# Kernel optimization log

Hardware: AMD Instinct MI355X
Metric: run time of the kernel (lower is better)

Reference implementation:

```python
import jax, jax.numpy as jnp
import numpy as np

NUM_NODES = 200000   # graph size
E = 128              # embedding_size
B = 256              # batch of target nodes
M = 8                # num_metapaths
L = 64               # walk length (number of (n1,n2,e) triples per metapath)
NUM_EDGE_TYPE = 8
H = 8                # num_heads (hardcoded in module)


def setup_inputs() -> dict:
    key = jax.random.key(0)
    ks = jax.random.split(key, 10)
    # walks: last dim = (n1, n2, edge_type)
    n12 = jax.random.randint(ks[0], (B, M, L, 2), 0, NUM_NODES)
    ety = jax.random.randint(ks[1], (B, M, L, 1), 0, NUM_EDGE_TYPE)
    node_mp_walks = jnp.concatenate([n12, ety], axis=-1)
    node_idx = jax.random.randint(ks[2], (B,), 0, NUM_NODES)
    mp_type_idx = jnp.arange(M)
    # fc1(onehot(n)) == node_table[n] + fc1_b  (node_table = fc1.weight.T)
    node_table = jax.random.normal(ks[3], (NUM_NODES, E), dtype=jnp.float32) * 0.1
    fc1_b = jnp.zeros((E,), dtype=jnp.float32)
    edge_table = jax.random.normal(ks[4], (NUM_EDGE_TYPE, E), dtype=jnp.float32) * 0.1
    # Indexed_LinearFC_List: one (E,E) linear per metapath
    W_mp = jax.random.normal(ks[5], (M, E, E), dtype=jnp.float32) * 0.05
    b_mp = jnp.zeros((M, E), dtype=jnp.float32)
    # MultiheadAttention params (embed_dim=E, num_heads=H, eval mode -> no dropout)
    Wqkv = jax.random.normal(ks[6], (3 * E, E), dtype=jnp.float32) * 0.05
    bqkv = jnp.zeros((3 * E,), dtype=jnp.float32)
    Wo = jax.random.normal(ks[7], (E, E), dtype=jnp.float32) * 0.05
    bo = jnp.zeros((E,), dtype=jnp.float32)
    return dict(node_idx=node_idx, mp_type_idx=mp_type_idx, node_mp_walks=node_mp_walks,
                node_table=node_table, fc1_b=fc1_b, edge_table=edge_table,
                W_mp=W_mp, b_mp=b_mp, Wqkv=Wqkv, bqkv=bqkv, Wo=Wo, bo=bo)


def reference(node_idx, mp_type_idx, node_mp_walks, node_table, fc1_b, edge_table,
              W_mp, b_mp, Wqkv, bqkv, Wo, bo):
    n1 = node_mp_walks[..., 0]          # [B,M,L]
    n2 = node_mp_walks[..., 1]
    e = node_mp_walks[..., 2]
    # gather node/edge embeddings (fc1 over one-hot == table row + bias)
    n1_vec = node_table[n1] + fc1_b     # [B,M,L,E]
    n2_vec = node_table[n2] + fc1_b     # [B,M,L,E]
    edge_vec = edge_table[e]            # [B,M,L,E]
    # elementwise fuse + mean over walk steps
    mp_agg_0 = jnp.mean(n1_vec * n2_vec * edge_vec, axis=2)        # [B,M,E]
    # per-metapath indexed linear
    Wsel = W_mp[mp_type_idx]            # [M,E,E]
    bsel = b_mp[mp_type_idx]            # [M,E]
    mp_agg_1 = jnp.einsum('bme,meo->bmo', mp_agg_0, Wsel) + bsel   # [B,M,E]
    # self-attention over metapaths (torch MHA, seq-first layout: [M,B,E])
    x = jnp.transpose(mp_agg_1, (1, 0, 2))                         # [M,B,E]
    qkv = x @ Wqkv.T + bqkv                                        # [M,B,3E]
    q, k, v = jnp.split(qkv, 3, axis=-1)
    hd = E // H
    q = q.reshape(M, B, H, hd)
    k = k.reshape(M, B, H, hd)
    v = v.reshape(M, B, H, hd)
    scores = jnp.einsum('mbhd,nbhd->bhmn', q, k) / jnp.sqrt(jnp.float32(hd))
    attn = jax.nn.softmax(scores, axis=-1)                         # [B,H,M,M]
    o = jnp.einsum('bhmn,nbhd->mbhd', attn, v).reshape(M, B, E)
    attn_output = o @ Wo.T + bo                                    # [M,B,E]
    return attn_output
```

## Files before the change

kernel.cpp:

```cpp
#include <hip/hip_runtime.h>

#define B 256
#define M 8
#define L 64
#define E 128
#define H 8
#define HD 16
#define NET 8
#define E3 384

__global__ __launch_bounds__(256) void k_transpose(
    const float* __restrict__ Wqkv, const float* __restrict__ Wo,
    float* __restrict__ WqkvT, float* __restrict__ WoT) {
  int idx = blockIdx.x * 256 + threadIdx.x;
  if (idx < E * E3) {
    int e = idx / E3;
    int o = idx - e * E3;
    WqkvT[idx] = Wqkv[o * E + e];
  } else {
    int j = idx - E * E3;
    int e = j >> 7, o = j & 127;
    WoT[j] = Wo[o * E + e];
  }
}

__global__ __launch_bounds__(256) void k_gather(
    const int* __restrict__ walks, const float* __restrict__ node_table,
    const float* __restrict__ fc1_b, const float* __restrict__ edge_table,
    float* __restrict__ agg0) {
  __shared__ int s_idx[L * 3];
  __shared__ float s_et[NET * E];
  __shared__ float4 s_red[256];

  int r = blockIdx.x;
  int t = threadIdx.x;
  int g = t >> 5, lane = t & 31;

  if (t < L * 3) s_idx[t] = walks[r * (L * 3) + t];
  for (int i = t; i < NET * E; i += 256) s_et[i] = edge_table[i];
  __syncthreads();

  const float4* nt4 = (const float4*)node_table;
  float4 fb = ((const float4*)fc1_b)[lane];
  float4 acc = make_float4(0.f, 0.f, 0.f, 0.f);

  #pragma unroll
  for (int i = 0; i < 8; ++i) {
    int l = (i << 3) + g;
    int n1 = s_idx[3 * l];
    int n2 = s_idx[3 * l + 1];
    int et = s_idx[3 * l + 2];
    float4 a = nt4[n1 * 32 + lane];
    float4 c = nt4[n2 * 32 + lane];
    float4 ev = ((const float4*)(s_et + et * E))[lane];
    acc.x += (a.x + fb.x) * (c.x + fb.x) * ev.x;
    acc.y += (a.y + fb.y) * (c.y + fb.y) * ev.y;
    acc.z += (a.z + fb.z) * (c.z + fb.z) * ev.z;
    acc.w += (a.w + fb.w) * (c.w + fb.w) * ev.w;
  }
  s_red[t] = acc;
  __syncthreads();
  if (t < 32) {
    float4 s = s_red[t];
    #pragma unroll
    for (int gg = 1; gg < 8; ++gg) {
      float4 v = s_red[gg * 32 + t];
      s.x += v.x; s.y += v.y; s.z += v.z; s.w += v.w;
    }
    const float inv = 1.0f / (float)L;
    s.x *= inv; s.y *= inv; s.z *= inv; s.w *= inv;
    ((float4*)agg0)[r * 32 + t] = s;
  }
}

__global__ __launch_bounds__(256) void k_mlp(
    const float* __restrict__ agg0, const int* __restrict__ mp_type_idx,
    const float* __restrict__ W_mp, const float* __restrict__ b_mp,
    const float* __restrict__ WqkvT, const float* __restrict__ bqkv,
    float* __restrict__ qkv) {
  __shared__ float xs[8][E];
  __shared__ float ys[8][E];
  int t = threadIdx.x;
  int m = blockIdx.y;
  int b0 = blockIdx.x * 8;
  int mp = mp_type_idx[m];
  int o = t & 127;
  int half = t >> 7;

  #pragma unroll
  for (int i = 0; i < 4; ++i) {
    int idx = i * 256 + t;
    int j = idx >> 7, e = idx & 127;
    xs[j][e] = agg0[((b0 + j) * M + m) * E + e];
  }
  __syncthreads();

  {
    const float* W = W_mp + mp * E * E;
    float acc[4] = {0, 0, 0, 0};
    for (int e = 0; e < E; ++e) {
      float w = W[e * E + o];
      #pragma unroll
      for (int j = 0; j < 4; ++j) acc[j] += xs[half * 4 + j][e] * w;
    }
    float bias = b_mp[mp * E + o];
    #pragma unroll
    for (int j = 0; j < 4; ++j) ys[half * 4 + j][o] = acc[j] + bias;
  }
  __syncthreads();

  #pragma unroll
  for (int c = 0; c < 3; ++c) {
    int oc = c * E + o;
    float acc[4] = {0, 0, 0, 0};
    for (int e = 0; e < E; ++e) {
      float w = WqkvT[e * E3 + oc];
      #pragma unroll
      for (int j = 0; j < 4; ++j) acc[j] += ys[half * 4 + j][e] * w;
    }
    float bias = bqkv[oc];
    #pragma unroll
    for (int j = 0; j < 4; ++j)
      qkv[((b0 + half * 4 + j) * M + m) * E3 + oc] = acc[j] + bias;
  }
}

__global__ __launch_bounds__(256) void k_attn(
    const float* __restrict__ qkv, const float* __restrict__ WoT,
    const float* __restrict__ bo, float* __restrict__ out) {
  __shared__ float s_qkv[M][E3 + 1];
  __shared__ float s_sc[H][M][M];
  __shared__ float s_o[M][E];
  int b = blockIdx.x;
  int t = threadIdx.x;

  #pragma unroll
  for (int i = 0; i < 12; ++i) {
    int idx = i * 256 + t;
    int mt = idx / E3;
    int col = idx - mt * E3;
    s_qkv[mt][col] = qkv[(b * M + mt) * E3 + col];
  }
  __syncthreads();

  #pragma unroll
  for (int i = 0; i < 2; ++i) {
    int idx = i * 256 + t;
    int h = idx >> 6;
    int mq = (idx >> 3) & 7;
    int n = idx & 7;
    float s = 0.f;
    #pragma unroll
    for (int d = 0; d < HD; ++d)
      s += s_qkv[mq][h * HD + d] * s_qkv[n][E + h * HD + d];
    s_sc[h][mq][n] = s * 0.25f;
  }
  __syncthreads();

  if (t < 64) {
    int h = t >> 3, mq = t & 7;
    float mx = -1e30f;
    #pragma unroll
    for (int n = 0; n < 8; ++n) mx = fmaxf(mx, s_sc[h][mq][n]);
    float ex[8];
    float sum = 0.f;
    #pragma unroll
    for (int n = 0; n < 8; ++n) { ex[n] = __expf(s_sc[h][mq][n] - mx); sum += ex[n]; }
    float inv = 1.0f / sum;
    #pragma unroll
    for (int n = 0; n < 8; ++n) s_sc[h][mq][n] = ex[n] * inv;
  }
  __syncthreads();

  #pragma unroll
  for (int i = 0; i < 4; ++i) {
    int idx = i * 256 + t;
    int mq = idx >> 7;
    int col = idx & 127;
    int h = col >> 4;
    float s = 0.f;
    #pragma unroll
    for (int n = 0; n < 8; ++n)
      s += s_sc[h][mq][n] * s_qkv[n][2 * E + col];
    s_o[mq][col] = s;
  }
  __syncthreads();

  int o = t & 127;
  int mbase = t >> 7;
  float accp[4] = {0, 0, 0, 0};
  for (int e = 0; e < E; ++e) {
    float w = WoT[e * E + o];
    #pragma unroll
    for (int i = 0; i < 4; ++i)
      accp[i] += s_o[2 * i + mbase][e] * w;
  }
  float bias = bo[o];
  #pragma unroll
  for (int i = 0; i < 4; ++i) {
    int mq = 2 * i + mbase;
    out[(mq * B + b) * E + o] = accp[i] + bias;
  }
}

extern "C" void kernel_launch(void* const* d_in, const int* in_sizes, int n_in,
                              void* d_out, int out_size, void* d_ws, size_t ws_size,
                              hipStream_t stream) {
  const int*   mp_type_idx = (const int*)d_in[1];
  const int*   walks       = (const int*)d_in[2];
  const float* node_table  = (const float*)d_in[3];
  const float* fc1_b       = (const float*)d_in[4];
  const float* edge_table  = (const float*)d_in[5];
  const float* W_mp        = (const float*)d_in[6];
  const float* b_mp        = (const float*)d_in[7];
  const float* Wqkv        = (const float*)d_in[8];
  const float* bqkv        = (const float*)d_in[9];
  const float* Wo          = (const float*)d_in[10];
  const float* bo          = (const float*)d_in[11];
  float* out = (float*)d_out;

  char* ws = (char*)d_ws;
  float* agg0  = (float*)(ws);
  float* qkvb  = (float*)(ws + (1 << 20));
  float* WqkvT = (float*)(ws + (4 << 20));
  float* WoT   = (float*)(ws + (4 << 20) + (256 << 10));

  k_transpose<<<dim3(256), dim3(256), 0, stream>>>(Wqkv, Wo, WqkvT, WoT);
  k_gather<<<dim3(B * M), dim3(256), 0, stream>>>(walks, node_table, fc1_b, edge_table, agg0);
  k_mlp<<<dim3(32, 8), dim3(256), 0, stream>>>(agg0, mp_type_idx, W_mp, b_mp, WqkvT, bqkv, qkvb);
  k_attn<<<dim3(B), dim3(256), 0, stream>>>(qkvb, WoT, bo, out);
}
```

Before: 208.2 us.

## Fuse gather, metapath linear, QKV projection and attention into one kernel

Merges the gather/mean, per-metapath linear, QKV projection and attention/output projection into a single kernel with one block per batch element, keeping intermediates in shared memory. This removes global round trips for agg0 and qkv and two kernel launches. The gather loop is restructured to issue eight independent row loads per step, increasing memory-level parallelism per thread. The trade-off is far fewer blocks (one per batch item) for the bandwidth-bound gather, which may reduce latency hiding, plus repeated weight reads per block.

```diff
diff --git a/kernel.cpp b/kernel.cpp
--- a/kernel.cpp
+++ b/kernel.cpp
@@ -24,122 +24,93 @@
   }
 }
 
-__global__ __launch_bounds__(256) void k_gather(
+__global__ __launch_bounds__(256) void k_fused(
     const int* __restrict__ walks, const float* __restrict__ node_table,
     const float* __restrict__ fc1_b, const float* __restrict__ edge_table,
-    float* __restrict__ agg0) {
-  __shared__ int s_idx[L * 3];
+    const int* __restrict__ mp_type_idx,
+    const float* __restrict__ W_mp, const float* __restrict__ b_mp,
+    const float* __restrict__ WqkvT, const float* __restrict__ bqkv,
+    const float* __restrict__ WoT, const float* __restrict__ bo,
+    float* __restrict__ out) {
+  __shared__ int   s_idx[M][L][3];
   __shared__ float s_et[NET * E];
-  __shared__ float4 s_red[256];
+  __shared__ float s_x[M][E];
+  __shared__ float s_y[M][E];
+  __shared__ float s_qkv[M][E3 + 1];
+  __shared__ float s_sc[H][M][M];
+  __shared__ float s_o[M][E];
+  __shared__ int   s_mp[M];
 
-  int r = blockIdx.x;
+  int b = blockIdx.x;
   int t = threadIdx.x;
   int g = t >> 5, lane = t & 31;
 
-  if (t < L * 3) s_idx[t] = walks[r * (L * 3) + t];
-  for (int i = t; i < NET * E; i += 256) s_et[i] = edge_table[i];
+  const int* wb = walks + b * (M * L * 3);
+  #pragma unroll
+  for (int i = 0; i < 6; ++i) ((int*)s_idx)[i * 256 + t] = wb[i * 256 + t];
+  #pragma unroll
+  for (int i = 0; i < 4; ++i) s_et[i * 256 + t] = edge_table[i * 256 + t];
+  if (t < M) s_mp[t] = mp_type_idx[t];
   __syncthreads();
 
   const float4* nt4 = (const float4*)node_table;
   float4 fb = ((const float4*)fc1_b)[lane];
-  float4 acc = make_float4(0.f, 0.f, 0.f, 0.f);
-
-  #pragma unroll
-  for (int i = 0; i < 8; ++i) {
-    int l = (i << 3) + g;
-    int n1 = s_idx[3 * l];
-    int n2 = s_idx[3 * l + 1];
-    int et = s_idx[3 * l + 2];
-    float4 a = nt4[n1 * 32 + lane];
-    float4 c = nt4[n2 * 32 + lane];
-    float4 ev = ((const float4*)(s_et + et * E))[lane];
-    acc.x += (a.x + fb.x) * (c.x + fb.x) * ev.x;
-    acc.y += (a.y + fb.y) * (c.y + fb.y) * ev.y;
-    acc.z += (a.z + fb.z) * (c.z + fb.z) * ev.z;
-    acc.w += (a.w + fb.w) * (c.w + fb.w) * ev.w;
-  }
-  s_red[t] = acc;
-  __syncthreads();
-  if (t < 32) {
-    float4 s = s_red[t];
-    #pragma unroll
-    for (int gg = 1; gg < 8; ++gg) {
-      float4 v = s_red[gg * 32 + t];
-      s.x += v.x; s.y += v.y; s.z += v.z; s.w += v.w;
+  {
+    float4 acc = make_float4(0.f, 0.f, 0.f, 0.f);
+    for (int l0 = 0; l0 < L; l0 += 8) {
+      float4 a[8], c[8];
+      #pragma unroll
+      for (int i = 0; i < 8; ++i) {
+        int n1 = s_idx[g][l0 + i][0];
+        int n2 = s_idx[g][l0 + i][1];
+        a[i] = nt4[n1 * 32 + lane];
+        c[i] = nt4[n2 * 32 + lane];
+      }
+      #pragma unroll
+      for (int i = 0; i < 8; ++i) {
+        int et = s_idx[g][l0 + i][2];
+        float4 ev = ((const float4*)(s_et + et * E))[lane];
+        acc.x += (a[i].x + fb.x) * (c[i].x + fb.x) * ev.x;
+        acc.y += (a[i].y + fb.y) * (c[i].y + fb.y) * ev.y;
+        acc.z += (a[i].z + fb.z) * (c[i].z + fb.z) * ev.z;
+        acc.w += (a[i].w + fb.w) * (c[i].w + fb.w) * ev.w;
+      }
     }
     const float inv = 1.0f / (float)L;
-    s.x *= inv; s.y *= inv; s.z *= inv; s.w *= inv;
-    ((float4*)agg0)[r * 32 + t] = s;
-  }
-}
-
-__global__ __launch_bounds__(256) void k_mlp(
-    const float* __restrict__ agg0, const int* __restrict__ mp_type_idx,
-    const float* __restrict__ W_mp, const float* __restrict__ b_mp,
-    const float* __restrict__ WqkvT, const float* __restrict__ bqkv,
-    float* __restrict__ qkv) {
-  __shared__ float xs[8][E];
-  __shared__ float ys[8][E];
-  int t = threadIdx.x;
-  int m = blockIdx.y;
-  int b0 = blockIdx.x * 8;
-  int mp = mp_type_idx[m];
-  int o = t & 127;
-  int half = t >> 7;
-
-  #pragma unroll
-  for (int i = 0; i < 4; ++i) {
-    int idx = i * 256 + t;
-    int j = idx >> 7, e = idx & 127;
-    xs[j][e] = agg0[((b0 + j) * M + m) * E + e];
+    acc.x *= inv; acc.y *= inv; acc.z *= inv; acc.w *= inv;
+    ((float4*)s_x[g])[lane] = acc;
   }
   __syncthreads();
 
   {
-    const float* W = W_mp + mp * E * E;
-    float acc[4] = {0, 0, 0, 0};
+    int mp = s_mp[g];
+    const float4* W4 = (const float4*)(W_mp + mp * E * E);
+    float4 acc = make_float4(0.f, 0.f, 0.f, 0.f);
     for (int e = 0; e < E; ++e) {
-      float w = W[e * E + o];
-      #pragma unroll
-      for (int j = 0; j < 4; ++j) acc[j] += xs[half * 4 + j][e] * w;
+      float x = s_x[g][e];
+      float4 w = W4[e * 32 + lane];
+      acc.x += x * w.x; acc.y += x * w.y; acc.z += x * w.z; acc.w += x * w.w;
     }
-    float bias = b_mp[mp * E + o];
-    #pragma unroll
-    for (int j = 0; j < 4; ++j) ys[half * 4 + j][o] = acc[j] + bias;
+    float4 bb = ((const float4*)(b_mp + mp * E))[lane];
+    acc.x += bb.x; acc.y += bb.y; acc.z += bb.z; acc.w += bb.w;
+    ((float4*)s_y[g])[lane] = acc;
   }
   __syncthreads();
 
   #pragma unroll
-  for (int c = 0; c < 3; ++c) {
-    int oc = c * E + o;
-    float acc[4] = {0, 0, 0, 0};
+  for (int p = 0; p < 3; ++p) {
+    float4 acc = make_float4(0.f, 0.f, 0.f, 0.f);
     for (int e = 0; e < E; ++e) {
-      float w = WqkvT[e * E3 + oc];
-      #pragma unroll
-      for (int j = 0; j < 4; ++j) acc[j] += ys[half * 4 + j][e] * w;
+      float x = s_y[g][e];
+      float4 w = ((const float4*)(WqkvT + e * E3))[p * 32 + lane];
+      acc.x += x * w.x; acc.y += x * w.y; acc.z += x * w.z; acc.w += x * w.w;
     }
-    float bias = bqkv[oc];
-    #pragma unroll
-    for (int j = 0; j < 4; ++j)
-      qkv[((b0 + half * 4 + j) * M + m) * E3 + oc] = acc[j] + bias;
-  }
-}
-
-__global__ __launch_bounds__(256) void k_attn(
-    const float* __restrict__ qkv, const float* __restrict__ WoT,
-    const float* __restrict__ bo, float* __restrict__ out) {
-  __shared__ float s_qkv[M][E3 + 1];
-  __shared__ float s_sc[H][M][M];
-  __shared__ float s_o[M][E];
-  int b = blockIdx.x;
-  int t = threadIdx.x;
-
-  #pragma unroll
-  for (int i = 0; i < 12; ++i) {
-    int idx = i * 256 + t;
-    int mt = idx / E3;
-    int col = idx - mt * E3;
-    s_qkv[mt][col] = qkv[(b * M + mt) * E3 + col];
+    float4 bb = ((const float4*)bqkv)[p * 32 + lane];
+    int base = p * 128 + lane * 4;
+    s_qkv[g][base + 0] = acc.x + bb.x;
+    s_qkv[g][base + 1] = acc.y + bb.y;
+    s_qkv[g][base + 2] = acc.z + bb.z;
+    s_qkv[g][base + 3] = acc.w + bb.w;
   }
   __syncthreads();
 
@@ -186,20 +157,17 @@
   }
   __syncthreads();
 
-  int o = t & 127;
-  int mbase = t >> 7;
-  float accp[4] = {0, 0, 0, 0};
-  for (int e = 0; e < E; ++e) {
-    float w = WoT[e * E + o];
-    #pragma unroll
-    for (int i = 0; i < 4; ++i)
-      accp[i] += s_o[2 * i + mbase][e] * w;
-  }
-  float bias = bo[o];
-  #pragma unroll
-  for (int i = 0; i < 4; ++i) {
-    int mq = 2 * i + mbase;
-    out[(mq * B + b) * E + o] = accp[i] + bias;
+  {
+    const float4* Wo4 = (const float4*)WoT;
+    float4 acc = make_float4(0.f, 0.f, 0.f, 0.f);
+    for (int e = 0; e < E; ++e) {
+      float x = s_o[g][e];
+      float4 w = Wo4[e * 32 + lane];
+      acc.x += x * w.x; acc.y += x * w.y; acc.z += x * w.z; acc.w += x * w.w;
+    }
+    float4 bb = ((const float4*)bo)[lane];
+    acc.x += bb.x; acc.y += bb.y; acc.z += bb.z; acc.w += bb.w;
+    ((float4*)(out + (g * B + b) * E))[lane] = acc;
   }
 }
 
@@ -220,13 +188,11 @@
   float* out = (float*)d_out;
 
   char* ws = (char*)d_ws;
-  float* agg0  = (float*)(ws);
-  float* qkvb  = (float*)(ws + (1 << 20));
-  float* WqkvT = (float*)(ws + (4 << 20));
-  float* WoT   = (float*)(ws + (4 << 20) + (256 << 10));
+  float* WqkvT = (float*)(ws);
+  float* WoT   = (float*)(ws + (256 << 10));
 
   k_transpose<<<dim3(256), dim3(256), 0, stream>>>(Wqkv, Wo, WqkvT, WoT);
-  k_gather<<<dim3(B * M), dim3(256), 0, stream>>>(walks, node_table, fc1_b, edge_table, agg0);
-  k_mlp<<<dim3(32, 8), dim3(256), 0, stream>>>(agg0, mp_type_idx, W_mp, b_mp, WqkvT, bqkv, qkvb);
-  k_attn<<<dim3(B), dim3(256), 0, stream>>>(qkvb, WoT, bo, out);
+  k_fused<<<dim3(B), dim3(256), 0, stream>>>(
+      walks, node_table, fc1_b, edge_table, mp_type_idx,
+      W_mp, b_mp, WqkvT, bqkv, WoT, bo, out);
 }
```

Measured after the change: 203.7 us. 1.02x faster.
